# Optimization experiments

Hardware: AMD Instinct MI355X
Metric: run time of the kernel (lower is better)

Reference implementation:

```python
import jax, jax.numpy as jnp
import numpy as np

B, T, W, L, H, TW = 2, 4096, 2048, 2048, 8, 4
HD = L // H  # head dim for block-diagonal gate projections


def setup_inputs() -> dict:
    key = jax.random.key(0)
    ks = jax.random.split(key, 16)
    inv_sqrt_w = 1.0 / np.sqrt(W)
    inv_sqrt_l = 1.0 / np.sqrt(L)
    inv_sqrt_hd = 1.0 / np.sqrt(HD)
    return {
        "x": jax.random.normal(ks[0], (B, T, W), dtype=jnp.float32),
        "segment_pos": jnp.tile(jnp.arange(T, dtype=jnp.int32), (B, 1)),
        # linear_y, linear_x: width -> lru_width
        "w_y": jax.random.normal(ks[1], (W, L), dtype=jnp.float32) * inv_sqrt_w,
        "b_y": jnp.zeros((L,), dtype=jnp.float32),
        "w_x": jax.random.normal(ks[2], (W, L), dtype=jnp.float32) * inv_sqrt_w,
        "b_x": jnp.zeros((L,), dtype=jnp.float32),
        # linear_out: lru_width -> width
        "w_out": jax.random.normal(ks[3], (L, W), dtype=jnp.float32) * inv_sqrt_l,
        "b_out": jnp.zeros((W,), dtype=jnp.float32),
        # depthwise causal temporal conv, kernel [TW, L]
        "conv_w": jax.random.normal(ks[4], (TW, L), dtype=jnp.float32) / np.sqrt(TW),
        "conv_b": jnp.zeros((L,), dtype=jnp.float32),
        # RG-LRU: a_param and two block-diagonal gate projections
        "a_param": jax.random.uniform(ks[5], (L,), dtype=jnp.float32, minval=-2.0, maxval=1.0),
        "igate_w": jax.random.normal(ks[6], (H, HD, HD), dtype=jnp.float32) * inv_sqrt_hd,
        "igate_b": jnp.zeros((H, HD), dtype=jnp.float32),
        "agate_w": jax.random.normal(ks[7], (H, HD, HD), dtype=jnp.float32) * inv_sqrt_hd,
        "agate_b": jnp.zeros((H, HD), dtype=jnp.float32),
    }


def _block_diag_linear(u, w, b):
    # u: [B,T,L] -> [B,T,H,HD] blockwise projected -> [B,T,L]
    uh = u.reshape(u.shape[0], u.shape[1], H, HD)
    y = jnp.einsum("bthd,hde->bthe", uh, w) + b
    return y.reshape(u.shape)


def _forward(x, segment_pos, w_y, b_y, w_x, b_x, w_out, b_out,
             conv_w, conv_b, a_param, igate_w, igate_b, agate_w, agate_b):
    # gate branch: linear_y + tanh-approx GELU
    y = jax.nn.gelu(jnp.einsum("btw,wl->btl", x, w_y) + b_y, approximate=True)
    # recurrent branch: linear_x
    xb = jnp.einsum("btw,wl->btl", x, w_x) + b_x
    # causal depthwise temporal conv (width TW), zero history before t=0
    x_pad = jnp.pad(xb, ((0, 0), (TW - 1, 0), (0, 0)))
    conv = conv_b + sum(conv_w[j] * x_pad[:, j:j + T] for j in range(TW))
    # RG-LRU gates
    gate_x = jax.nn.sigmoid(_block_diag_linear(conv, igate_w, igate_b))
    gate_a = jax.nn.sigmoid(_block_diag_linear(conv, agate_w, agate_b))
    log_a = -8.0 * gate_a * jax.nn.softplus(a_param)  # [B,T,L]
    a = jnp.exp(log_a)
    reset = (segment_pos == 0)[..., None]  # [B,T,1]
    multiplier = jnp.sqrt(1.0 - jnp.exp(2.0 * log_a))
    multiplier = jnp.where(reset, 1.0, multiplier)
    normed = conv * gate_x * multiplier
    a_masked = jnp.where(reset, 0.0, a)
    # diagonal linear recurrence: h_t = a_t * h_{t-1} + normed_t
    def step(h, inp):
        a_t, x_t = inp
        h = a_t * h + x_t
        return h, h
    h0 = jnp.zeros((x.shape[0], L), dtype=x.dtype)
    _, hs = jax.lax.scan(step, h0, (a_masked.transpose(1, 0, 2), normed.transpose(1, 0, 2)))
    hs = hs.transpose(1, 0, 2)  # [B,T,L]
    # elementwise gate then output projection
    return jnp.einsum("btl,lw->btw", hs * y, w_out) + b_out


def reference(x, segment_pos, w_y, b_y, w_x, b_x, w_out, b_out,
              conv_w, conv_b, a_param, igate_w, igate_b, agate_w, agate_b):
    return _forward(x, segment_pos, w_y, b_y, w_x, b_x, w_out, b_out,
                    conv_w, conv_b, a_param, igate_w, igate_b, agate_w, agate_b)
```

## Files before the change

kernel.cpp:

```cpp
#include <hip/hip_runtime.h>
#include <cstdint>
#include <math.h>

typedef _Float16 f16;
typedef f16 f16x8 __attribute__((ext_vector_type(8)));
typedef f16 f16x4 __attribute__((ext_vector_type(4)));
typedef float f32x4 __attribute__((ext_vector_type(4)));

#define BATCH 2
#define TSEQ 4096
#define WID 2048
#define LRU 2048
#define NHEAD 8
#define HDIM 256
#define MTOT (BATCH * TSEQ)
#define CT 128
#define NC (TSEQ / CT)

__device__ __forceinline__ void gl2lds16(const f16* g, f16* l) {
  __builtin_amdgcn_global_load_lds(
      (__attribute__((address_space(1))) uint32_t*)(uintptr_t)g,
      (__attribute__((address_space(3))) uint32_t*)(uint32_t)(uintptr_t)l,
      16, 0, 0);
}

__device__ __forceinline__ float fast_rcp(float x) {
  float r; asm("v_rcp_f32 %0, %1" : "=v"(r) : "v"(x)); return r;
}
__device__ __forceinline__ float fast_sigmoid(float x) {
  return fast_rcp(1.f + __expf(-x));
}
__device__ __forceinline__ float f16bits_to_f(uint32_t b) {
  return (float)__builtin_bit_cast(f16, (uint16_t)b);
}

__global__ void prep_kernel(const float* __restrict__ x, f16* __restrict__ Xh,
                            const float* __restrict__ w_y, const float* __restrict__ w_x,
                            const float* __restrict__ w_out,
                            f16* __restrict__ wyT, f16* __restrict__ wxT, f16* __restrict__ woutT,
                            const float* __restrict__ ig, const float* __restrict__ ag,
                            f16* __restrict__ igT, f16* __restrict__ agT,
                            const float* __restrict__ ap, float* __restrict__ spT) {
  __shared__ float tile[32][33];
  const int bid = blockIdx.x, t = threadIdx.x;
  if (bid < 16384) {
    int i = bid * 256 + t;
    float4 v = ((const float4*)x)[i];
    f16x4 o = { (f16)v.x, (f16)v.y, (f16)v.z, (f16)v.w };
    ((f16x4*)Xh)[i] = o;
    return;
  }
  if (bid >= 29696) {
    int i = (bid - 29696) * 256 + t;
    spT[i] = log1pf(expf(ap[i]));
    return;
  }
  const int tx = t & 31, ty = t >> 5;
  const float* ib; f16* ob; int R, C, c0, r0;
  if (bid < 28672) {
    int idx = bid - 16384;
    int z = idx >> 12, tl = idx & 4095;
    ib = z == 0 ? w_y : (z == 1 ? w_x : w_out);
    ob = z == 0 ? wyT : (z == 1 ? wxT : woutT);
    R = 2048; C = 2048;
    c0 = (tl & 63) * 32; r0 = (tl >> 6) * 32;
  } else {
    int idx = bid - 28672;
    int z = idx >> 6, tl = idx & 63;
    ib = (z < 8 ? ig : ag) + (long long)(z & 7) * HDIM * HDIM;
    ob = (z < 8 ? igT : agT) + (long long)(z & 7) * HDIM * HDIM;
    R = HDIM; C = HDIM;
    c0 = (tl & 7) * 32; r0 = (tl >> 3) * 32;
  }
#pragma unroll
  for (int i = 0; i < 32; i += 8)
    tile[ty + i][tx] = ib[(long long)(r0 + ty + i) * C + c0 + tx];
  __syncthreads();
#pragma unroll
  for (int i = 0; i < 32; i += 8)
    ob[(long long)(c0 + ty + i) * R + r0 + tx] = (f16)tile[tx][ty + i];
}

template <int MODE>
__global__ __launch_bounds__(256, 4) void gemm_128(
    const f16* __restrict__ A, const f16* __restrict__ BT,
    const float* __restrict__ bias, void* __restrict__ Cout,
    int M, int N, int K) {
  __shared__ __align__(16) f16 As[128 * 64];
  __shared__ __align__(16) f16 Bs[128 * 64];
  const int m0 = blockIdx.x * 128, n0 = blockIdx.y * 128;
  const int t = threadIdx.x;
  const int lane = t & 63, wave = t >> 6;
  const int wr = (wave >> 1) * 64, wc = (wave & 1) * 64;
  const int l15 = lane & 15, quad = lane >> 4;
  const int srow = t >> 3;
  const int sg = ((t & 7) ^ (srow & 7)) * 8;

  const f16* Ag = A + (long long)(m0 + srow) * K + sg;
  const f16* Bg = BT + (long long)(n0 + srow) * K + sg;
  const long long r32 = (long long)32 * K;

  f32x4 c[4][4] = {};
  const int NT = K >> 6;
  for (int kt = 0; kt < NT; ++kt) {
    const f16* a = Ag + kt * 64;
    const f16* b = Bg + kt * 64;
#pragma unroll
    for (int cc = 0; cc < 4; ++cc) {
      gl2lds16(a + cc * r32, &As[cc * 2048 + t * 8]);
      gl2lds16(b + cc * r32, &Bs[cc * 2048 + t * 8]);
    }
    __syncthreads();
    f16x8 af[4][2], bf[4][2];
#pragma unroll
    for (int f = 0; f < 4; ++f) {
#pragma unroll
      for (int kh = 0; kh < 2; ++kh) {
        const int sa = ((kh * 4 + quad) ^ (l15 & 7)) * 8;
        af[f][kh] = *(const f16x8*)&As[(wr + f * 16 + l15) * 64 + sa];
        bf[f][kh] = *(const f16x8*)&Bs[(wc + f * 16 + l15) * 64 + sa];
      }
    }
#pragma unroll
    for (int kh = 0; kh < 2; ++kh)
#pragma unroll
      for (int i = 0; i < 4; ++i)
#pragma unroll
        for (int j = 0; j < 4; ++j)
          c[i][j] = __builtin_amdgcn_mfma_f32_16x16x32_f16(af[i][kh], bf[j][kh], c[i][j], 0, 0, 0);
    __syncthreads();
  }
#pragma unroll
  for (int i = 0; i < 4; ++i) {
#pragma unroll
    for (int j = 0; j < 4; ++j) {
      const int col = n0 + wc + j * 16 + l15;
      const float bv = bias[col];
      const int row0 = m0 + wr + i * 16 + quad * 4;
#pragma unroll
      for (int r = 0; r < 4; ++r) {
        float v = c[i][j][r] + bv;
        long long off = (long long)(row0 + r) * N + col;
        if constexpr (MODE == 0) {
          float z2 = 1.5957691216057308f * (v + 0.044715f * v * v * v);
          ((f16*)Cout)[off] = (f16)(v * fast_sigmoid(z2));
        } else if constexpr (MODE == 1) {
          ((f16*)Cout)[off] = (f16)v;
        } else {
          ((float*)Cout)[off] = v;
        }
      }
    }
  }
}

__global__ __launch_bounds__(512, 2) void gates_fused(
    const f16* __restrict__ XBh, const float* __restrict__ cw, const float* __restrict__ cb,
    const f16* __restrict__ BiT, const f16* __restrict__ BaT,
    const float* __restrict__ ib, const float* __restrict__ ab,
    const float* __restrict__ spT, const int* __restrict__ segpos,
    uint32_t* __restrict__ AN, float* __restrict__ Ac, float* __restrict__ Hc) {
  __shared__ __align__(16) f16 As[128 * 256];
  __shared__ __align__(16) f16 Bi[256 * 32];
  __shared__ __align__(16) f16 Ba[256 * 32];
  const int m0 = blockIdx.x * 128;
  const int h = blockIdx.y;
  const int ncol0 = h * HDIM;
  const int t = threadIdx.x;
  const int lane = t & 63, wave = t >> 6;
  const int wr = (wave >> 2) * 64;
  const int wc = (wave & 3) * 64;
  const int l15 = lane & 15, quad = lane >> 4;

  const int srow = t >> 2, scol = (t & 3) * 8;
  const f16* Big = BiT + (long long)(ncol0 + srow) * HDIM + scol;
  const f16* Bag = BaT + (long long)(ncol0 + srow) * HDIM + scol;
  gl2lds16(Big, &Bi[t * 8]);
  gl2lds16(Big + (long long)128 * HDIM, &Bi[128 * 32 + t * 8]);
  gl2lds16(Bag, &Ba[t * 8]);
  gl2lds16(Bag + (long long)128 * HDIM, &Ba[128 * 32 + t * 8]);

#pragma unroll 4
  for (int it = 0; it < 8; ++it) {
    int idx = it * 512 + t;
    int r = idx >> 5, kc = idx & 31;
    int m = m0 + r, tpos = m & (TSEQ - 1);
    int colbase = ncol0 + kc * 8;
    float acc[8];
    {
      float4 c0 = *(const float4*)&cb[colbase];
      float4 c1 = *(const float4*)&cb[colbase + 4];
      acc[0] = c0.x; acc[1] = c0.y; acc[2] = c0.z; acc[3] = c0.w;
      acc[4] = c1.x; acc[5] = c1.y; acc[6] = c1.z; acc[7] = c1.w;
    }
#pragma unroll
    for (int d = 0; d < 4; ++d) {
      if (tpos >= d) {
        f16x8 xv = *(const f16x8*)&XBh[(long long)(m - d) * LRU + colbase];
        float4 w0 = *(const float4*)&cw[(3 - d) * LRU + colbase];
        float4 w1 = *(const float4*)&cw[(3 - d) * LRU + colbase + 4];
        acc[0] += w0.x * (float)xv[0]; acc[1] += w0.y * (float)xv[1];
        acc[2] += w0.z * (float)xv[2]; acc[3] += w0.w * (float)xv[3];
        acc[4] += w1.x * (float)xv[4]; acc[5] += w1.y * (float)xv[5];
        acc[6] += w1.z * (float)xv[6]; acc[7] += w1.w * (float)xv[7];
      }
    }
    f16x8 o;
#pragma unroll
    for (int k = 0; k < 8; ++k) o[k] = (f16)acc[k];
    int gs = (kc & ~7) | ((kc ^ r) & 7);
    *(f16x8*)&As[r * 256 + gs * 8] = o;
  }
  __syncthreads();

  f32x4 ci[4][4] = {};
  f32x4 ca[4][4] = {};
  for (int k0 = 0; k0 < HDIM; k0 += 32) {
    f16x8 af[4], bif[4], baf[4];
#pragma unroll
    for (int i = 0; i < 4; ++i) {
      int row = wr + i * 16 + l15;
      int g = (k0 >> 3) + quad;
      int gsw = (g & ~7) | ((g ^ row) & 7);
      af[i] = *(const f16x8*)&As[row * 256 + gsw * 8];
    }
#pragma unroll
    for (int j = 0; j < 4; ++j) {
      bif[j] = *(const f16x8*)&Bi[(wc + j * 16 + l15) * 32 + quad * 8];
      baf[j] = *(const f16x8*)&Ba[(wc + j * 16 + l15) * 32 + quad * 8];
    }
#pragma unroll
    for (int i = 0; i < 4; ++i)
#pragma unroll
      for (int j = 0; j < 4; ++j) {
        ci[i][j] = __builtin_amdgcn_mfma_f32_16x16x32_f16(af[i], bif[j], ci[i][j], 0, 0, 0);
        ca[i][j] = __builtin_amdgcn_mfma_f32_16x16x32_f16(af[i], baf[j], ca[i][j], 0, 0, 0);
      }
    __syncthreads();
    if (k0 + 32 < HDIM) {
      const f16* bi2 = Big + (k0 + 32);
      const f16* ba2 = Bag + (k0 + 32);
      gl2lds16(bi2, &Bi[t * 8]);
      gl2lds16(bi2 + (long long)128 * HDIM, &Bi[128 * 32 + t * 8]);
      gl2lds16(ba2, &Ba[t * 8]);
      gl2lds16(ba2 + (long long)128 * HDIM, &Ba[128 * 32 + t * 8]);
      __syncthreads();
    }
  }

  const int mb = m0 >> 12;
  const int cch = (m0 & (TSEQ - 1)) >> 7;
  uint32_t rsmask = 0;
#pragma unroll
  for (int i = 0; i < 4; ++i) {
    int4 sp4 = *(const int4*)&segpos[m0 + wr + i * 16 + quad * 4];
    rsmask |= (sp4.x == 0 ? 1u : 0u) << (i * 4 + 0);
    rsmask |= (sp4.y == 0 ? 1u : 0u) << (i * 4 + 1);
    rsmask |= (sp4.z == 0 ? 1u : 0u) << (i * 4 + 2);
    rsmask |= (sp4.w == 0 ? 1u : 0u) << (i * 4 + 3);
  }
  float Aw[4], hw[4];
#pragma unroll
  for (int j = 0; j < 4; ++j) {
    const int cl = wc + j * 16 + l15;
    const int col = ncol0 + cl;
    const float ibv = ib[col], abv = ab[col];
    const float sp = spT[col];
    float A4[4], h4[4];
#pragma unroll
    for (int i = 0; i < 4; ++i) {
      float Aseg = 1.f, hseg = 0.f;
#pragma unroll
      for (int r = 0; r < 4; ++r) {
        const int rowL = wr + i * 16 + quad * 4 + r;
        const int row = m0 + rowL;
        float gx = fast_sigmoid(ci[i][j][r] + ibv);
        float ga = fast_sigmoid(ca[i][j][r] + abv);
        float la = -8.f * ga * sp;
        bool rs = (rsmask >> (i * 4 + r)) & 1u;
        float a = rs ? 0.f : __expf(la);
        uint32_t afx = __float2uint_rn(a * 65536.f);
        if (afx > 65535u) afx = 65535u;
        float aq = (float)afx * (1.f / 65536.f);
        int g = cl >> 3, e = cl & 7;
        int gsw = (g & ~7) | ((g ^ rowL) & 7);
        float cv = (float)As[rowL * 256 + gsw * 8 + e];
        float mult = rs ? 1.f : sqrtf(fmaxf(1.f - aq * aq, 0.f));
        f16 nh = (f16)(cv * gx * mult);
        AN[(long long)row * LRU + col] =
            afx | ((uint32_t)__builtin_bit_cast(uint16_t, nh) << 16);
        float xq = (float)nh;
        hseg = aq * hseg + xq;
        Aseg *= aq;
      }
      A4[i] = Aseg; h4[i] = hseg;
    }
#pragma unroll
    for (int i = 0; i < 4; ++i) {
      float A = A4[i], hv = h4[i];
#pragma unroll
      for (int d = 1; d <= 2; d <<= 1) {
        int src = quad >= d ? lane - 16 * d : lane;
        float Ap = __shfl(A, src);
        float hp = __shfl(hv, src);
        if (quad >= d) { hv = A * hp + hv; A = Ap * A; }
      }
      A4[i] = __shfl(A, 48 + l15);
      h4[i] = __shfl(hv, 48 + l15);
    }
    float Awv = 1.f, hwv = 0.f;
#pragma unroll
    for (int i = 0; i < 4; ++i) { hwv = A4[i] * hwv + h4[i]; Awv *= A4[i]; }
    Aw[j] = Awv; hw[j] = hwv;
  }
  float* carry = (float*)Bi;
  __syncthreads();
  if (wr == 0 && quad == 0) {
#pragma unroll
    for (int j = 0; j < 4; ++j) {
      int cl = wc + j * 16 + l15;
      carry[cl * 2] = Aw[j]; carry[cl * 2 + 1] = hw[j];
    }
  }
  __syncthreads();
  if (wr == 64 && quad == 0) {
#pragma unroll
    for (int j = 0; j < 4; ++j) {
      int cl = wc + j * 16 + l15;
      float At = carry[cl * 2], ht = carry[cl * 2 + 1];
      float A = At * Aw[j];
      float hv = Aw[j] * ht + hw[j];
      int o = (mb * NC + cch) * LRU + ncol0 + cl;
      Ac[o] = A; Hc[o] = hv;
    }
  }
}

__global__ void scan23_kernel(const uint32_t* __restrict__ AN,
                              const float* __restrict__ Ac, const float* __restrict__ Hc,
                              const f16* __restrict__ Yh, f16* __restrict__ G) {
  const int l = (blockIdx.x * 256 + threadIdx.x) * 2;
  const int c = blockIdx.y, b = blockIdx.z;
  float h0 = 0.f, h1 = 0.f;
  for (int cc = 0; cc < c; ++cc) {
    const int o = (b * NC + cc) * LRU + l;
    const float2 A2 = *(const float2*)&Ac[o];
    const float2 H2 = *(const float2*)&Hc[o];
    h0 = A2.x * h0 + H2.x;
    h1 = A2.y * h1 + H2.y;
  }
  long long base = ((long long)b * TSEQ + (long long)c * CT) * LRU + l;
#pragma unroll 8
  for (int s = 0; s < CT; ++s) {
    const long long o = base + (long long)s * LRU;
    const uint2 p = *(const uint2*)&AN[o];
    const uint32_t yb = *(const uint32_t*)&Yh[o];
    const float a0 = (float)(p.x & 0xFFFFu) * (1.f / 65536.f);
    const float x0 = f16bits_to_f(p.x >> 16);
    const float a1 = (float)(p.y & 0xFFFFu) * (1.f / 65536.f);
    const float x1 = f16bits_to_f(p.y >> 16);
    h0 = a0 * h0 + x0;
    h1 = a1 * h1 + x1;
    const f16 g0 = (f16)(h0 * f16bits_to_f(yb & 0xFFFFu));
    const f16 g1 = (f16)(h1 * f16bits_to_f(yb >> 16));
    *(uint32_t*)&G[o] = ((uint32_t)__builtin_bit_cast(uint16_t, g1) << 16)
                        | (uint32_t)__builtin_bit_cast(uint16_t, g0);
  }
}

extern "C" void kernel_launch(void* const* d_in, const int* in_sizes, int n_in,
                              void* d_out, int out_size, void* d_ws, size_t ws_size,
                              hipStream_t stream) {
  (void)in_sizes; (void)n_in; (void)out_size; (void)ws_size;
  const float* x          = (const float*)d_in[0];
  const int*   segment_pos= (const int*)d_in[1];
  const float* w_y        = (const float*)d_in[2];
  const float* b_y        = (const float*)d_in[3];
  const float* w_x        = (const float*)d_in[4];
  const float* b_x        = (const float*)d_in[5];
  const float* w_out      = (const float*)d_in[6];
  const float* b_out      = (const float*)d_in[7];
  const float* conv_w     = (const float*)d_in[8];
  const float* conv_b     = (const float*)d_in[9];
  const float* a_param    = (const float*)d_in[10];
  const float* igate_w    = (const float*)d_in[11];
  const float* igate_b    = (const float*)d_in[12];
  const float* agate_w    = (const float*)d_in[13];
  const float* agate_b    = (const float*)d_in[14];
  float* out = (float*)d_out;

  char* base = (char*)d_ws;
  size_t off = 0;
  auto alloc = [&](size_t nbytes) -> void* {
    void* p = base + off;
    off = (off + nbytes + 255) & ~(size_t)255;
    return p;
  };
  f16*     Xh    = (f16*)alloc((size_t)MTOT * LRU * 2);
  f16*     Yh    = (f16*)alloc((size_t)MTOT * LRU * 2);
  f16*     XBh   = (f16*)alloc((size_t)MTOT * LRU * 2);
  uint32_t* AN   = (uint32_t*)alloc((size_t)MTOT * LRU * 4);
  f16*     wyT   = (f16*)alloc((size_t)WID * LRU * 2);
  f16*     wxT   = (f16*)alloc((size_t)WID * LRU * 2);
  f16*     woutT = (f16*)alloc((size_t)LRU * WID * 2);
  f16*     igwT  = (f16*)alloc((size_t)NHEAD * HDIM * HDIM * 2);
  f16*     agwT  = (f16*)alloc((size_t)NHEAD * HDIM * HDIM * 2);
  float*   Ac    = (float*)alloc((size_t)BATCH * NC * LRU * 4);
  float*   Hc    = (float*)alloc((size_t)BATCH * NC * LRU * 4);
  float*   spT   = (float*)alloc((size_t)LRU * 4);
  f16*     G     = Xh;

  prep_kernel<<<29704, 256, 0, stream>>>(x, Xh, w_y, w_x, w_out, wyT, wxT, woutT,
                                         igate_w, agate_w, igwT, agwT, a_param, spT);
  gemm_128<0><<<dim3(MTOT / 128, LRU / 128), 256, 0, stream>>>(
      Xh, wyT, b_y, Yh, MTOT, LRU, WID);
  gemm_128<1><<<dim3(MTOT / 128, LRU / 128), 256, 0, stream>>>(
      Xh, wxT, b_x, XBh, MTOT, LRU, WID);
  gates_fused<<<dim3(MTOT / 128, NHEAD), 512, 0, stream>>>(
      XBh, conv_w, conv_b, igwT, agwT, igate_b, agate_b, spT, segment_pos, AN, Ac, Hc);
  scan23_kernel<<<dim3(LRU / 512, NC, BATCH), 256, 0, stream>>>(AN, Ac, Hc, Yh, G);
  gemm_128<2><<<dim3(MTOT / 128, WID / 128), 256, 0, stream>>>(
      G, woutT, b_out, out, MTOT, WID, LRU);
}
```

Measured before the change: 487.0 us.

## Shrink gates_fused chunk to 64 rows with 4 waves, dropping cross-wave carry merge

Result: no change. 494.6 us (+1.6%).

```diff
diff --git a/kernel.cpp b/kernel.cpp
--- a/kernel.cpp
+++ b/kernel.cpp
@@ -14,7 +14,7 @@
 #define NHEAD 8
 #define HDIM 256
 #define MTOT (BATCH * TSEQ)
-#define CT 128
+#define CT 64
 #define NC (TSEQ / CT)
 
 __device__ __forceinline__ void gl2lds16(const f16* g, f16* l) {
@@ -154,35 +154,35 @@
   }
 }
 
-__global__ __launch_bounds__(512, 2) void gates_fused(
+__global__ __launch_bounds__(256, 2) void gates_fused(
     const f16* __restrict__ XBh, const float* __restrict__ cw, const float* __restrict__ cb,
     const f16* __restrict__ BiT, const f16* __restrict__ BaT,
     const float* __restrict__ ib, const float* __restrict__ ab,
     const float* __restrict__ spT, const int* __restrict__ segpos,
     uint32_t* __restrict__ AN, float* __restrict__ Ac, float* __restrict__ Hc) {
-  __shared__ __align__(16) f16 As[128 * 256];
+  __shared__ __align__(16) f16 As[64 * 256];
   __shared__ __align__(16) f16 Bi[256 * 32];
   __shared__ __align__(16) f16 Ba[256 * 32];
-  const int m0 = blockIdx.x * 128;
+  const int m0 = blockIdx.x * 64;
   const int h = blockIdx.y;
   const int ncol0 = h * HDIM;
   const int t = threadIdx.x;
   const int lane = t & 63, wave = t >> 6;
-  const int wr = (wave >> 2) * 64;
-  const int wc = (wave & 3) * 64;
+  const int wc = wave * 64;
   const int l15 = lane & 15, quad = lane >> 4;
 
   const int srow = t >> 2, scol = (t & 3) * 8;
   const f16* Big = BiT + (long long)(ncol0 + srow) * HDIM + scol;
   const f16* Bag = BaT + (long long)(ncol0 + srow) * HDIM + scol;
-  gl2lds16(Big, &Bi[t * 8]);
-  gl2lds16(Big + (long long)128 * HDIM, &Bi[128 * 32 + t * 8]);
-  gl2lds16(Bag, &Ba[t * 8]);
-  gl2lds16(Bag + (long long)128 * HDIM, &Ba[128 * 32 + t * 8]);
+#pragma unroll
+  for (int q = 0; q < 4; ++q) {
+    gl2lds16(Big + (long long)(q * 64) * HDIM, &Bi[q * 64 * 32 + t * 8]);
+    gl2lds16(Bag + (long long)(q * 64) * HDIM, &Ba[q * 64 * 32 + t * 8]);
+  }
 
 #pragma unroll 4
   for (int it = 0; it < 8; ++it) {
-    int idx = it * 512 + t;
+    int idx = it * 256 + t;
     int r = idx >> 5, kc = idx & 31;
     int m = m0 + r, tpos = m & (TSEQ - 1);
     int colbase = ncol0 + kc * 8;
@@ -219,7 +219,7 @@
     f16x8 af[4], bif[4], baf[4];
 #pragma unroll
     for (int i = 0; i < 4; ++i) {
-      int row = wr + i * 16 + l15;
+      int row = i * 16 + l15;
       int g = (k0 >> 3) + quad;
       int gsw = (g & ~7) | ((g ^ row) & 7);
       af[i] = *(const f16x8*)&As[row * 256 + gsw * 8];
@@ -240,26 +240,26 @@
     if (k0 + 32 < HDIM) {
       const f16* bi2 = Big + (k0 + 32);
       const f16* ba2 = Bag + (k0 + 32);
-      gl2lds16(bi2, &Bi[t * 8]);
-      gl2lds16(bi2 + (long long)128 * HDIM, &Bi[128 * 32 + t * 8]);
-      gl2lds16(ba2, &Ba[t * 8]);
-      gl2lds16(ba2 + (long long)128 * HDIM, &Ba[128 * 32 + t * 8]);
+#pragma unroll
+      for (int q = 0; q < 4; ++q) {
+        gl2lds16(bi2 + (long long)(q * 64) * HDIM, &Bi[q * 64 * 32 + t * 8]);
+        gl2lds16(ba2 + (long long)(q * 64) * HDIM, &Ba[q * 64 * 32 + t * 8]);
+      }
       __syncthreads();
     }
   }
 
   const int mb = m0 >> 12;
-  const int cch = (m0 & (TSEQ - 1)) >> 7;
+  const int cch = (m0 & (TSEQ - 1)) >> 6;
   uint32_t rsmask = 0;
 #pragma unroll
   for (int i = 0; i < 4; ++i) {
-    int4 sp4 = *(const int4*)&segpos[m0 + wr + i * 16 + quad * 4];
+    int4 sp4 = *(const int4*)&segpos[m0 + i * 16 + quad * 4];
     rsmask |= (sp4.x == 0 ? 1u : 0u) << (i * 4 + 0);
     rsmask |= (sp4.y == 0 ? 1u : 0u) << (i * 4 + 1);
     rsmask |= (sp4.z == 0 ? 1u : 0u) << (i * 4 + 2);
     rsmask |= (sp4.w == 0 ? 1u : 0u) << (i * 4 + 3);
   }
-  float Aw[4], hw[4];
 #pragma unroll
   for (int j = 0; j < 4; ++j) {
     const int cl = wc + j * 16 + l15;
@@ -272,7 +272,7 @@
       float Aseg = 1.f, hseg = 0.f;
 #pragma unroll
       for (int r = 0; r < 4; ++r) {
-        const int rowL = wr + i * 16 + quad * 4 + r;
+        const int rowL = i * 16 + quad * 4 + r;
         const int row = m0 + rowL;
         float gx = fast_sigmoid(ci[i][j][r] + ibv);
         float ga = fast_sigmoid(ca[i][j][r] + abv);
@@ -311,27 +311,9 @@
     float Awv = 1.f, hwv = 0.f;
 #pragma unroll
     for (int i = 0; i < 4; ++i) { hwv = A4[i] * hwv + h4[i]; Awv *= A4[i]; }
-    Aw[j] = Awv; hw[j] = hwv;
-  }
-  float* carry = (float*)Bi;
-  __syncthreads();
-  if (wr == 0 && quad == 0) {
-#pragma unroll
-    for (int j = 0; j < 4; ++j) {
-      int cl = wc + j * 16 + l15;
-      carry[cl * 2] = Aw[j]; carry[cl * 2 + 1] = hw[j];
-    }
-  }
-  __syncthreads();
-  if (wr == 64 && quad == 0) {
-#pragma unroll
-    for (int j = 0; j < 4; ++j) {
-      int cl = wc + j * 16 + l15;
-      float At = carry[cl * 2], ht = carry[cl * 2 + 1];
-      float A = At * Aw[j];
-      float hv = Aw[j] * ht + hw[j];
-      int o = (mb * NC + cch) * LRU + ncol0 + cl;
-      Ac[o] = A; Hc[o] = hv;
+    if (quad == 0) {
+      int o = (mb * NC + cch) * LRU + col;
+      Ac[o] = Awv; Hc[o] = hwv;
     }
   }
 }
@@ -416,7 +398,7 @@
       Xh, wyT, b_y, Yh, MTOT, LRU, WID);
   gemm_128<1><<<dim3(MTOT / 128, LRU / 128), 256, 0, stream>>>(
       Xh, wxT, b_x, XBh, MTOT, LRU, WID);
-  gates_fused<<<dim3(MTOT / 128, NHEAD), 512, 0, stream>>>(
+  gates_fused<<<dim3(MTOT / 64, NHEAD), 256, 0, stream>>>(
       XBh, conv_w, conv_b, igwT, agwT, igate_b, agate_b, spT, segment_pos, AN, Ac, Hc);
   scan23_kernel<<<dim3(LRU / 512, NC, BATCH), 256, 0, stream>>>(AN, Ac, Hc, Yh, G);
   gemm_128<2><<<dim3(MTOT / 128, WID / 128), 256, 0, stream>>>(
```

## Halve scan chunk size and vectorize weight transpose in prep kernel

Applied to the files above, without the earlier changes.

New measurement: 501.5 us. 3.0% more time.

```diff
diff --git a/kernel.cpp b/kernel.cpp
--- a/kernel.cpp
+++ b/kernel.cpp
@@ -14,8 +14,8 @@
 #define NHEAD 8
 #define HDIM 256
 #define MTOT (BATCH * TSEQ)
-#define CT 128
-#define NC (TSEQ / CT)
+#define CTH 64
+#define NCH (TSEQ / CTH)
 
 __device__ __forceinline__ void gl2lds16(const f16* g, f16* l) {
   __builtin_amdgcn_global_load_lds(
@@ -41,7 +41,7 @@
                             const float* __restrict__ ig, const float* __restrict__ ag,
                             f16* __restrict__ igT, f16* __restrict__ agT,
                             const float* __restrict__ ap, float* __restrict__ spT) {
-  __shared__ float tile[32][33];
+  __shared__ float tile[64][65];
   const int bid = blockIdx.x, t = threadIdx.x;
   if (bid < 16384) {
     int i = bid * 256 + t;
@@ -50,35 +50,51 @@
     ((f16x4*)Xh)[i] = o;
     return;
   }
-  if (bid >= 29696) {
-    int i = (bid - 29696) * 256 + t;
+  if (bid >= 19712) {
+    int i = (bid - 19712) * 256 + t;
     spT[i] = log1pf(expf(ap[i]));
     return;
   }
-  const int tx = t & 31, ty = t >> 5;
   const float* ib; f16* ob; int R, C, c0, r0;
-  if (bid < 28672) {
+  if (bid < 19456) {
     int idx = bid - 16384;
-    int z = idx >> 12, tl = idx & 4095;
+    int z = idx >> 10, tl = idx & 1023;
     ib = z == 0 ? w_y : (z == 1 ? w_x : w_out);
     ob = z == 0 ? wyT : (z == 1 ? wxT : woutT);
     R = 2048; C = 2048;
-    c0 = (tl & 63) * 32; r0 = (tl >> 6) * 32;
+    c0 = (tl & 31) * 64; r0 = (tl >> 5) * 64;
   } else {
-    int idx = bid - 28672;
-    int z = idx >> 6, tl = idx & 63;
+    int idx = bid - 19456;
+    int z = idx >> 4, tl = idx & 15;
     ib = (z < 8 ? ig : ag) + (long long)(z & 7) * HDIM * HDIM;
     ob = (z < 8 ? igT : agT) + (long long)(z & 7) * HDIM * HDIM;
     R = HDIM; C = HDIM;
-    c0 = (tl & 7) * 32; r0 = (tl >> 3) * 32;
-  }
-#pragma unroll
-  for (int i = 0; i < 32; i += 8)
-    tile[ty + i][tx] = ib[(long long)(r0 + ty + i) * C + c0 + tx];
+    c0 = (tl & 3) * 64; r0 = (tl >> 2) * 64;
+  }
+  {
+    const int rl = t >> 2, q = t & 3;
+    const float* src = ib + (long long)(r0 + rl) * C + c0 + q * 16;
+#pragma unroll
+    for (int i = 0; i < 4; ++i) {
+      float4 v = *(const float4*)(src + i * 4);
+      int cc = q * 16 + i * 4;
+      tile[cc + 0][rl] = v.x; tile[cc + 1][rl] = v.y;
+      tile[cc + 2][rl] = v.z; tile[cc + 3][rl] = v.w;
+    }
+  }
   __syncthreads();
-#pragma unroll
-  for (int i = 0; i < 32; i += 8)
-    ob[(long long)(c0 + ty + i) * R + r0 + tx] = (f16)tile[tx][ty + i];
+  {
+    const int w = t & 31, cb = t >> 5;
+    uint32_t* o32 = (uint32_t*)ob;
+#pragma unroll
+    for (int i = 0; i < 8; ++i) {
+      int cl = cb + i * 8;
+      float x0 = tile[cl][2 * w], x1 = tile[cl][2 * w + 1];
+      uint32_t pk = (uint32_t)__builtin_bit_cast(uint16_t, (f16)x0)
+                  | ((uint32_t)__builtin_bit_cast(uint16_t, (f16)x1) << 16);
+      o32[((long long)(c0 + cl) * R + r0) / 2 + w] = pk;
+    }
+  }
 }
 
 template <int MODE>
@@ -249,7 +265,6 @@
   }
 
   const int mb = m0 >> 12;
-  const int cch = (m0 & (TSEQ - 1)) >> 7;
   uint32_t rsmask = 0;
 #pragma unroll
   for (int i = 0; i < 4; ++i) {
@@ -259,7 +274,7 @@
     rsmask |= (sp4.z == 0 ? 1u : 0u) << (i * 4 + 2);
     rsmask |= (sp4.w == 0 ? 1u : 0u) << (i * 4 + 3);
   }
-  float Aw[4], hw[4];
+  const int hcIdx = ((m0 & (TSEQ - 1)) >> 6) + (wr >> 6);
 #pragma unroll
   for (int j = 0; j < 4; ++j) {
     const int cl = wc + j * 16 + l15;
@@ -311,47 +326,30 @@
     float Awv = 1.f, hwv = 0.f;
 #pragma unroll
     for (int i = 0; i < 4; ++i) { hwv = A4[i] * hwv + h4[i]; Awv *= A4[i]; }
-    Aw[j] = Awv; hw[j] = hwv;
-  }
-  float* carry = (float*)Bi;
-  __syncthreads();
-  if (wr == 0 && quad == 0) {
-#pragma unroll
-    for (int j = 0; j < 4; ++j) {
-      int cl = wc + j * 16 + l15;
-      carry[cl * 2] = Aw[j]; carry[cl * 2 + 1] = hw[j];
-    }
-  }
-  __syncthreads();
-  if (wr == 64 && quad == 0) {
-#pragma unroll
-    for (int j = 0; j < 4; ++j) {
-      int cl = wc + j * 16 + l15;
-      float At = carry[cl * 2], ht = carry[cl * 2 + 1];
-      float A = At * Aw[j];
-      float hv = Aw[j] * ht + hw[j];
-      int o = (mb * NC + cch) * LRU + ncol0 + cl;
-      Ac[o] = A; Hc[o] = hv;
-    }
-  }
-}
-
-__global__ void scan23_kernel(const uint32_t* __restrict__ AN,
-                              const float* __restrict__ Ac, const float* __restrict__ Hc,
-                              const f16* __restrict__ Yh, f16* __restrict__ G) {
+    if (quad == 0) {
+      int o = (mb * NCH + hcIdx) * LRU + col;
+      Ac[o] = Awv; Hc[o] = hwv;
+    }
+  }
+}
+
+__global__ __launch_bounds__(256) void scan23_kernel(
+    const uint32_t* __restrict__ AN,
+    const float* __restrict__ Ac, const float* __restrict__ Hc,
+    const f16* __restrict__ Yh, f16* __restrict__ G) {
   const int l = (blockIdx.x * 256 + threadIdx.x) * 2;
   const int c = blockIdx.y, b = blockIdx.z;
   float h0 = 0.f, h1 = 0.f;
   for (int cc = 0; cc < c; ++cc) {
-    const int o = (b * NC + cc) * LRU + l;
+    const int o = (b * NCH + cc) * LRU + l;
     const float2 A2 = *(const float2*)&Ac[o];
     const float2 H2 = *(const float2*)&Hc[o];
     h0 = A2.x * h0 + H2.x;
     h1 = A2.y * h1 + H2.y;
   }
-  long long base = ((long long)b * TSEQ + (long long)c * CT) * LRU + l;
+  long long base = ((long long)b * TSEQ + (long long)c * CTH) * LRU + l;
 #pragma unroll 8
-  for (int s = 0; s < CT; ++s) {
+  for (int s = 0; s < CTH; ++s) {
     const long long o = base + (long long)s * LRU;
     const uint2 p = *(const uint2*)&AN[o];
     const uint32_t yb = *(const uint32_t*)&Yh[o];
@@ -405,12 +403,12 @@
   f16*     woutT = (f16*)alloc((size_t)LRU * WID * 2);
   f16*     igwT  = (f16*)alloc((size_t)NHEAD * HDIM * HDIM * 2);
   f16*     agwT  = (f16*)alloc((size_t)NHEAD * HDIM * HDIM * 2);
-  float*   Ac    = (float*)alloc((size_t)BATCH * NC * LRU * 4);
-  float*   Hc    = (float*)alloc((size_t)BATCH * NC * LRU * 4);
+  float*   Ac    = (float*)alloc((size_t)BATCH * NCH * LRU * 4);
+  float*   Hc    = (float*)alloc((size_t)BATCH * NCH * LRU * 4);
   float*   spT   = (float*)alloc((size_t)LRU * 4);
   f16*     G     = Xh;
 
-  prep_kernel<<<29704, 256, 0, stream>>>(x, Xh, w_y, w_x, w_out, wyT, wxT, woutT,
+  prep_kernel<<<19720, 256, 0, stream>>>(x, Xh, w_y, w_x, w_out, wyT, wxT, woutT,
                                          igate_w, agate_w, igwT, agwT, a_param, spT);
   gemm_128<0><<<dim3(MTOT / 128, LRU / 128), 256, 0, stream>>>(
       Xh, wyT, b_y, Yh, MTOT, LRU, WID);
@@ -418,7 +416,7 @@
       Xh, wxT, b_x, XBh, MTOT, LRU, WID);
   gates_fused<<<dim3(MTOT / 128, NHEAD), 512, 0, stream>>>(
       XBh, conv_w, conv_b, igwT, agwT, igate_b, agate_b, spT, segment_pos, AN, Ac, Hc);
-  scan23_kernel<<<dim3(LRU / 512, NC, BATCH), 256, 0, stream>>>(AN, Ac, Hc, Yh, G);
+  scan23_kernel<<<dim3(LRU / 512, NCH, BATCH), 256, 0, stream>>>(AN, Ac, Hc, Yh, G);
   gemm_128<2><<<dim3(MTOT / 128, WID / 128), 256, 0, stream>>>(
       G, woutT, b_out, out, MTOT, WID, LRU);
 }
```
